# Kernel tuning notes

Measured on AMD Instinct MI355X. Metric: run time of the kernel, lower is better.

The kernel has to match this reference:

```python
import jax, jax.numpy as jnp
import numpy as np

N_A = 3
N_CLS = 80
IGNORE_THRE = 0.6
EPS = 1e-7


def _pairwise_iou_cxcywh(a, b):
    # a: [..., M, 4], b: [..., N, 4] in (cx, cy, w, h) -> IoU [..., M, N]
    a_xy, a_wh = a[..., :, None, :2], a[..., :, None, 2:4]
    b_xy, b_wh = b[..., None, :, :2], b[..., None, :, 2:4]
    tl = jnp.maximum(a_xy - a_wh * 0.5, b_xy - b_wh * 0.5)
    br = jnp.minimum(a_xy + a_wh * 0.5, b_xy + b_wh * 0.5)
    inter = jnp.prod(jnp.clip(br - tl, 0.0), axis=-1)
    area_a = a_wh[..., 0] * a_wh[..., 1]
    area_b = b_wh[..., 0] * b_wh[..., 1]
    return inter / jnp.maximum(area_a + area_b - inter, 1e-16)


def _bce(p, t):
    p = jnp.clip(p, EPS, 1.0 - EPS)
    return -(t * jnp.log(p) + (1.0 - t) * jnp.log(1.0 - p))


def _yolo_loss(raw, labels, anchors_all, anchor_indices, img_size):
    nB = raw.shape[0]
    nG = raw.shape[2]
    nCH = 5 + N_CLS
    K = labels.shape[1]
    sg = jax.lax.stop_gradient

    # decode raw: (B, A*CH, G, G) -> (B, A, G, G, CH)
    raw = jnp.transpose(raw.reshape(nB, N_A, nCH, nG, nG), (0, 1, 3, 4, 2))
    xy_offset = jax.nn.sigmoid(raw[..., 0:2])            # (B,A,G,G,2)
    wh_scale = raw[..., 2:4]                             # (B,A,G,G,2)
    conf = jax.nn.sigmoid(raw[..., 4])                   # (B,A,G,G)
    classes = jax.nn.sigmoid(raw[..., 5:])               # (B,A,G,G,ncls)

    anchors = anchors_all[anchor_indices]                # (3,2), pixels
    g = jnp.arange(nG, dtype=raw.dtype)
    xs = g[None, None, None, :]
    ys = g[None, None, :, None]

    # detached decoded predictions, normalized to [0,1]
    px = (sg(xy_offset[..., 0]) + xs) / nG
    py = (sg(xy_offset[..., 1]) + ys) / nG
    pw = jnp.minimum(jnp.exp(sg(wh_scale[..., 0])) * anchors[:, 0][None, :, None, None] / img_size, 1.0)
    ph = jnp.minimum(jnp.exp(sg(wh_scale[..., 1])) * anchors[:, 1][None, :, None, None] / img_size, 1.0)
    pred_boxes = jnp.stack([px, py, pw, ph], axis=-1).reshape(nB, -1, 4)  # (B, A*G*G, 4)

    # labels: (B, K, 5) = [cls, xc, yc, w, h]; targets are constants
    labels = sg(labels)
    nlabel = jnp.sum(jnp.sum(labels, axis=2) > 0, axis=1)                 # (B,)
    valid_k = jnp.arange(K)[None, :] < nlabel[:, None]                    # (B,K)
    tcls = labels[..., 0].astype(jnp.int32)
    tx = labels[..., 1] * nG
    ty = labels[..., 2] * nG
    tw = labels[..., 3]
    th = labels[..., 4]
    ti = tx.astype(jnp.int32)
    tj = ty.astype(jnp.int32)

    # anchor matching on centered (0,0,w,h) boxes against all 9 anchors
    anch00 = jnp.concatenate([jnp.zeros_like(anchors_all), anchors_all / img_size], axis=1)  # (9,4)
    gt00 = jnp.stack([jnp.zeros_like(tw), jnp.zeros_like(tw), tw, th], axis=-1)              # (B,K,4)
    a_ious = _pairwise_iou_cxcywh(gt00, anch00[None])                                        # (B,K,9)
    best_n_all = jnp.argmax(a_ious, axis=-1)                                                 # (B,K)
    valid_anchor = jnp.any(best_n_all[..., None] == anchor_indices[None, None, :], axis=-1)
    valid = valid_k & valid_anchor                                                           # (B,K)
    best_n = best_n_all % N_A

    # ignore mask: preds whose best IoU against any (valid) gt exceeds threshold
    gt_boxes = jnp.stack([tx / nG, ty / nG, tw, th], axis=-1) * valid_k[..., None].astype(raw.dtype)
    pred_ious = _pairwise_iou_cxcywh(pred_boxes, gt_boxes)               # (B, A*G*G, K)
    ignore = (jnp.max(pred_ious, axis=-1) > IGNORE_THRE).reshape(nB, N_A, nG, nG)
    penalty_mask = ~ignore

    # scatter gt assignments; invalid rows dropped via OOB batch index
    b_idx = jnp.broadcast_to(jnp.arange(nB)[:, None], (nB, K))
    b_s = jnp.where(valid, b_idx, nB)

    obj_mask = jnp.zeros((nB, N_A, nG, nG), dtype=bool).at[b_s, best_n, tj, ti].set(True, mode='drop')
    penalty_mask = penalty_mask.at[b_s, best_n, tj, ti].set(True, mode='drop')

    naw = anchors / img_size                                             # (3,2)
    tgt_vals = jnp.stack([
        tx - jnp.floor(tx),
        ty - jnp.floor(ty),
        jnp.log(tw / naw[best_n, 0] + 1e-16),
        jnp.log(th / naw[best_n, 1] + 1e-16),
    ], axis=-1)                                                          # (B,K,4)
    target4 = jnp.zeros((nB, N_A, nG, nG, 4), raw.dtype).at[b_s, best_n, tj, ti].set(tgt_vals, mode='drop')
    tgt_scale = jnp.zeros((nB, N_A, nG, nG), raw.dtype).at[b_s, best_n, tj, ti].set(
        jnp.sqrt(2.0 - tw * th), mode='drop')
    tcls_oh = jnp.zeros((nB, N_A, nG, nG, N_CLS), raw.dtype).at[b_s, best_n, tj, ti, tcls].set(1.0, mode='drop')

    obj_f = obj_mask.astype(raw.dtype)
    pen_f = penalty_mask.astype(raw.dtype)
    w2 = tgt_scale * tgt_scale                                           # (B,A,G,G)

    loss_xy = jnp.sum(obj_f[..., None] * w2[..., None] * _bce(xy_offset, target4[..., 0:2]))
    loss_wh = jnp.sum(obj_f[..., None] * w2[..., None] * jnp.square(wh_scale - target4[..., 2:4]))
    loss_obj = jnp.sum(pen_f * _bce(conf, obj_f))
    loss_cls = jnp.sum(obj_f[..., None] * _bce(classes, tcls_oh))
    return loss_xy + 0.5 * loss_wh + loss_obj + loss_cls


def setup_inputs() -> dict:
    key = jax.random.key(0)
    k1, k2, k3, k4 = jax.random.split(key, 4)
    nB, K, nG = 16, 50, 76
    raw = jax.random.normal(k1, (nB, N_A * (5 + N_CLS), nG, nG), jnp.float32) * 0.5
    cls = jax.random.randint(k2, (nB, K), 0, N_CLS).astype(jnp.float32)
    xy = jax.random.uniform(k3, (nB, K, 2), jnp.float32, 0.02, 0.98)
    wh = jax.random.uniform(k4, (nB, K, 2), jnp.float32, 0.02, 0.4)
    labels = jnp.concatenate([cls[..., None], xy, wh], axis=-1)
    # make per-image label counts < K (rows of zeros are "no label")
    labels = labels * (jnp.arange(K) < 40).astype(jnp.float32)[None, :, None]
    anchors_all = jnp.array([[10, 13], [16, 30], [33, 23], [30, 61], [62, 45],
                             [59, 119], [116, 90], [156, 198], [373, 326]], jnp.float32)
    anchor_indices = jnp.array([0, 1, 2], jnp.int32)
    return {"raw": raw, "labels": labels, "anchors_all": anchors_all,
            "anchor_indices": anchor_indices, "img_size": 608}


def reference(raw, labels, anchors_all, anchor_indices, img_size):
    return _yolo_loss(raw, labels, anchors_all, anchor_indices, img_size)
```

## Files before the change

kernel.cpp:

```cpp
#include <hip/hip_runtime.h>
#include <math.h>

#define NB   16
#define KL   50
#define NG   76
#define NA   3
#define NCLS 80
#define NCH  85
#define GG   (NG*NG)
#define CELLS (NA*GG)
#define LOSS_BX ((CELLS + 255) / 256)
#define NPART (LOSS_BX * NB)

__device__ __forceinline__ float softplusf(float x) {
    float t = __expf(-fabsf(x));
    return fmaxf(x, 0.0f) + __logf(1.0f + t);
}

__global__ __launch_bounds__(256) void yolo_fused(
    const float* __restrict__ raw,
    const float* __restrict__ labels,
    const float* __restrict__ anchors_all,
    const int*   __restrict__ anchor_indices,
    const int*   __restrict__ img_size_p,
    float* __restrict__ partials)
{
    const int b = blockIdx.y;

    __shared__ float4 s_box[KL];
    __shared__ float  s_c[KL];
    __shared__ int    s_meta[KL];
    __shared__ float  s_tgt[KL][4];
    __shared__ float  s_w2[KL];
    __shared__ int    s_tc[KL];
    __shared__ float  s_red[4];

    const float img = (float)img_size_p[0];
    const float inv_img = __builtin_amdgcn_rcpf(img);

    if (threadIdx.x < 64) {
        const int k = threadIdx.x;
        int has = 0;
        float cls = 0.f, tx = 0.f, ty = 0.f, tw = 0.f, th = 0.f;
        if (k < KL) {
            const float* L = labels + ((size_t)b * KL + k) * 5;
            cls = L[0];
            tw = L[3]; th = L[4];
            has = ((cls + L[1] + L[2] + tw + th) > 0.0f) ? 1 : 0;
            tx = L[1] * (float)NG;
            ty = L[2] * (float)NG;
        }
        unsigned long long bal = __ballot(has);
        int nlabel = __popcll(bal);

        if (k < KL) {
            int valid_k = (k < nlabel) ? 1 : 0;

            float best = -1.0f; int bestn = 0;
            float area_t = tw * th;
            for (int n = 0; n < 9; ++n) {
                float aw = anchors_all[2 * n + 0] * inv_img;
                float ah = anchors_all[2 * n + 1] * inv_img;
                float inter = fmaxf(fminf(tw, aw), 0.0f) * fmaxf(fminf(th, ah), 0.0f);
                float iou = inter / fmaxf(area_t + aw * ah - inter, 1e-16f);
                if (iou > best) { best = iou; bestn = n; }
            }
            int va = 0;
            for (int t = 0; t < 3; ++t) va |= (bestn == anchor_indices[t]) ? 1 : 0;
            int bn = bestn % NA;
            int ti = (int)tx, tj = (int)ty;
            int valid = valid_k && va && (ti >= 0) && (ti < NG) && (tj >= 0) && (tj < NG);
            s_meta[k] = valid ? (bn * GG + tj * NG + ti) : -1;

            float vkf = valid_k ? 1.0f : 0.0f;
            float gx = tx * (1.0f / (float)NG) * vkf;
            float gy = ty * (1.0f / (float)NG) * vkf;
            float gw = tw * vkf, gh = th * vkf;
            s_box[k] = make_float4(gx - 0.5f * gw, gy - 0.5f * gh,
                                   gx + 0.5f * gw, gy + 0.5f * gh);
            s_c[k] = 0.375f * (gw * gh);

            float naw = anchors_all[anchor_indices[bn] * 2 + 0] * inv_img;
            float nah = anchors_all[anchor_indices[bn] * 2 + 1] * inv_img;
            s_tgt[k][0] = tx - floorf(tx);
            s_tgt[k][1] = ty - floorf(ty);
            s_tgt[k][2] = __logf(tw / naw + 1e-16f);
            s_tgt[k][3] = __logf(th / nah + 1e-16f);
            s_w2[k] = 2.0f - tw * th;
            s_tc[k] = (int)cls;
        }
    }
    __syncthreads();

    const int c0 = blockIdx.x * 256 + threadIdx.x;
    const bool live = c0 < CELLS;
    const int c = live ? c0 : 0;

    const int a = c / GG;
    const int r = c - a * GG;
    const int j = r / NG;
    const int i = r - j * NG;
    const float* R = raw + ((size_t)(b * NA + a) * NCH) * GG + r;

    float rx = R[0],      ry = R[GG];
    float rw = R[2 * GG], rh = R[3 * GG];
    float rc = R[4 * GG];

    float sx = __builtin_amdgcn_rcpf(1.0f + __expf(-rx));
    float sy = __builtin_amdgcn_rcpf(1.0f + __expf(-ry));

    int ai = anchor_indices[a];
    float aw = anchors_all[2 * ai + 0] * inv_img;
    float ah = anchors_all[2 * ai + 1] * inv_img;

    float px = (sx + (float)i) * (1.0f / (float)NG);
    float py = (sy + (float)j) * (1.0f / (float)NG);
    float pw = fminf(__expf(rw) * aw, 1.0f);
    float ph = fminf(__expf(rh) * ah, 1.0f);

    float tA = 0.375f * (pw * ph);
    float ax0 = px - 0.5f * pw, ax1 = px + 0.5f * pw;
    float ay0 = py - 0.5f * ph, ay1 = py + 0.5f * ph;

    float margin = -1.0f;
    int kobj = -1;
    #pragma unroll 10
    for (int k = 0; k < KL; ++k) {
        float4 g = s_box[k];
        float iw = fminf(ax1, g.z) - fmaxf(ax0, g.x);
        float ih = fminf(ay1, g.w) - fmaxf(ay0, g.y);
        float inter = fmaxf(iw, 0.0f) * fmaxf(ih, 0.0f);
        margin = fmaxf(margin, inter - s_c[k]);
        kobj = (s_meta[k] == c) ? k : kobj;
    }
    bool ignore = margin > tA;
    bool obj = (kobj >= 0) && live;

    float loss = 0.0f;
    if (obj || !ignore)
        loss = softplusf(rc) - (obj ? rc : 0.0f);

    if (obj) {
        float w2 = s_w2[kobj];
        float t0 = s_tgt[kobj][0], t1 = s_tgt[kobj][1];
        float t2 = s_tgt[kobj][2], t3 = s_tgt[kobj][3];
        loss += w2 * ((softplusf(rx) - t0 * rx) + (softplusf(ry) - t1 * ry));
        float dw = rw - t2, dh = rh - t3;
        loss += 0.5f * w2 * (dw * dw + dh * dh);
        int tc = s_tc[kobj];
        float cl = 0.0f;
        #pragma unroll 8
        for (int cc = 0; cc < NCLS; ++cc) {
            float z = R[(5 + cc) * GG];
            cl += softplusf(z);
            if (cc == tc) cl -= z;
        }
        loss += cl;
    }
    if (!live) loss = 0.0f;

    for (int off = 32; off > 0; off >>= 1)
        loss += __shfl_down(loss, off, 64);
    if ((threadIdx.x & 63) == 0) s_red[threadIdx.x >> 6] = loss;
    __syncthreads();
    if (threadIdx.x == 0)
        partials[(size_t)blockIdx.y * gridDim.x + blockIdx.x] =
            s_red[0] + s_red[1] + s_red[2] + s_red[3];
}

__global__ __launch_bounds__(256) void yolo_finalize(
    const float* __restrict__ partials, float* __restrict__ out)
{
    float s = 0.0f;
    for (int i = threadIdx.x; i < NPART; i += 256) s += partials[i];
    for (int off = 32; off > 0; off >>= 1)
        s += __shfl_down(s, off, 64);
    __shared__ float red[4];
    if ((threadIdx.x & 63) == 0) red[threadIdx.x >> 6] = s;
    __syncthreads();
    if (threadIdx.x == 0) out[0] = red[0] + red[1] + red[2] + red[3];
}

extern "C" void kernel_launch(void* const* d_in, const int* in_sizes, int n_in,
                              void* d_out, int out_size, void* d_ws, size_t ws_size,
                              hipStream_t stream) {
    const float* raw            = (const float*)d_in[0];
    const float* labels         = (const float*)d_in[1];
    const float* anchors_all    = (const float*)d_in[2];
    const int*   anchor_indices = (const int*)d_in[3];
    const int*   img_size_p     = (const int*)d_in[4];
    float* out = (float*)d_out;

    float* partials = (float*)d_ws;

    dim3 grid(LOSS_BX, NB);
    yolo_fused<<<grid, 256, 0, stream>>>(raw, labels, anchors_all,
                                         anchor_indices, img_size_p, partials);
    yolo_finalize<<<1, 256, 0, stream>>>(partials, out);
}
```

Measured before the change: 142.5 us.

## Process four cells per thread with float4 loads and 64-thread blocks

Each thread now handles four consecutive grid cells, loading the box and confidence channels as float4 vectors and reusing each shared-memory label read across four cells in the IoU loop. Blocks shrink to a single 64-lane wavefront, so the label preprocessing runs on every thread and the cross-wave shared reduction and its barrier go away. The intent is fewer LDS reads per cell and wider global loads. In exchange, per-thread register use rises, and the class-loss loop for object cells still reads channels with strided scalar loads. Because GG (5776) is a multiple of 4, the float4 loads stay aligned and four consecutive cells never cross an anchor plane.

```diff
diff --git a/kernel.cpp b/kernel.cpp
--- a/kernel.cpp
+++ b/kernel.cpp
@@ -9,7 +9,10 @@
 #define NCH  85
 #define GG   (NG*NG)
 #define CELLS (NA*GG)
-#define LOSS_BX ((CELLS + 255) / 256)
+#define CPT  4
+#define TPB  64
+#define CPB  (TPB*CPT)
+#define LOSS_BX ((CELLS + CPB - 1) / CPB)
 #define NPART (LOSS_BX * NB)
 
 __device__ __forceinline__ float softplusf(float x) {
@@ -17,7 +20,7 @@
     return fmaxf(x, 0.0f) + __logf(1.0f + t);
 }
 
-__global__ __launch_bounds__(256) void yolo_fused(
+__global__ __launch_bounds__(64) void yolo_fused(
     const float* __restrict__ raw,
     const float* __restrict__ labels,
     const float* __restrict__ anchors_all,
@@ -30,15 +33,14 @@
     __shared__ float4 s_box[KL];
     __shared__ float  s_c[KL];
     __shared__ int    s_meta[KL];
-    __shared__ float  s_tgt[KL][4];
+    __shared__ float4 s_tgt[KL];
     __shared__ float  s_w2[KL];
     __shared__ int    s_tc[KL];
-    __shared__ float  s_red[4];
 
     const float img = (float)img_size_p[0];
     const float inv_img = __builtin_amdgcn_rcpf(img);
 
-    if (threadIdx.x < 64) {
+    {
         const int k = threadIdx.x;
         int has = 0;
         float cls = 0.f, tx = 0.f, ty = 0.f, tw = 0.f, th = 0.f;
@@ -82,90 +84,106 @@
 
             float naw = anchors_all[anchor_indices[bn] * 2 + 0] * inv_img;
             float nah = anchors_all[anchor_indices[bn] * 2 + 1] * inv_img;
-            s_tgt[k][0] = tx - floorf(tx);
-            s_tgt[k][1] = ty - floorf(ty);
-            s_tgt[k][2] = __logf(tw / naw + 1e-16f);
-            s_tgt[k][3] = __logf(th / nah + 1e-16f);
+            s_tgt[k] = make_float4(tx - floorf(tx), ty - floorf(ty),
+                                   __logf(tw / naw + 1e-16f),
+                                   __logf(th / nah + 1e-16f));
             s_w2[k] = 2.0f - tw * th;
             s_tc[k] = (int)cls;
         }
     }
     __syncthreads();
 
-    const int c0 = blockIdx.x * 256 + threadIdx.x;
+    const int c0 = blockIdx.x * CPB + threadIdx.x * CPT;
     const bool live = c0 < CELLS;
-    const int c = live ? c0 : 0;
-
-    const int a = c / GG;
-    const int r = c - a * GG;
+    const int cb = live ? c0 : 0;
+
+    const int a = cb / GG;
+    const int r = cb - a * GG;
     const int j = r / NG;
     const int i = r - j * NG;
     const float* R = raw + ((size_t)(b * NA + a) * NCH) * GG + r;
 
-    float rx = R[0],      ry = R[GG];
-    float rw = R[2 * GG], rh = R[3 * GG];
-    float rc = R[4 * GG];
-
-    float sx = __builtin_amdgcn_rcpf(1.0f + __expf(-rx));
-    float sy = __builtin_amdgcn_rcpf(1.0f + __expf(-ry));
+    float4 rx4 = *(const float4*)(R);
+    float4 ry4 = *(const float4*)(R + GG);
+    float4 rw4 = *(const float4*)(R + 2 * GG);
+    float4 rh4 = *(const float4*)(R + 3 * GG);
+    float4 rc4 = *(const float4*)(R + 4 * GG);
 
     int ai = anchor_indices[a];
     float aw = anchors_all[2 * ai + 0] * inv_img;
     float ah = anchors_all[2 * ai + 1] * inv_img;
 
-    float px = (sx + (float)i) * (1.0f / (float)NG);
-    float py = (sy + (float)j) * (1.0f / (float)NG);
-    float pw = fminf(__expf(rw) * aw, 1.0f);
-    float ph = fminf(__expf(rh) * ah, 1.0f);
-
-    float tA = 0.375f * (pw * ph);
-    float ax0 = px - 0.5f * pw, ax1 = px + 0.5f * pw;
-    float ay0 = py - 0.5f * ph, ay1 = py + 0.5f * ph;
-
-    float margin = -1.0f;
-    int kobj = -1;
-    #pragma unroll 10
+    float rxv[CPT] = {rx4.x, rx4.y, rx4.z, rx4.w};
+    float ryv[CPT] = {ry4.x, ry4.y, ry4.z, ry4.w};
+    float rwv[CPT] = {rw4.x, rw4.y, rw4.z, rw4.w};
+    float rhv[CPT] = {rh4.x, rh4.y, rh4.z, rh4.w};
+    float rcv[CPT] = {rc4.x, rc4.y, rc4.z, rc4.w};
+
+    float ax0[CPT], ax1[CPT], ay0[CPT], ay1[CPT], tA[CPT], margin[CPT];
+    int kobj[CPT];
+    #pragma unroll
+    for (int cc = 0; cc < CPT; ++cc) {
+        float sx = __builtin_amdgcn_rcpf(1.0f + __expf(-rxv[cc]));
+        float sy = __builtin_amdgcn_rcpf(1.0f + __expf(-ryv[cc]));
+        float px = (sx + (float)(i + cc)) * (1.0f / (float)NG);
+        float py = (sy + (float)j) * (1.0f / (float)NG);
+        float pw = fminf(__expf(rwv[cc]) * aw, 1.0f);
+        float ph = fminf(__expf(rhv[cc]) * ah, 1.0f);
+        tA[cc] = 0.375f * (pw * ph);
+        ax0[cc] = px - 0.5f * pw; ax1[cc] = px + 0.5f * pw;
+        ay0[cc] = py - 0.5f * ph; ay1[cc] = py + 0.5f * ph;
+        margin[cc] = -1.0f;
+        kobj[cc] = -1;
+    }
+
+    #pragma unroll 5
     for (int k = 0; k < KL; ++k) {
         float4 g = s_box[k];
-        float iw = fminf(ax1, g.z) - fmaxf(ax0, g.x);
-        float ih = fminf(ay1, g.w) - fmaxf(ay0, g.y);
-        float inter = fmaxf(iw, 0.0f) * fmaxf(ih, 0.0f);
-        margin = fmaxf(margin, inter - s_c[k]);
-        kobj = (s_meta[k] == c) ? k : kobj;
-    }
-    bool ignore = margin > tA;
-    bool obj = (kobj >= 0) && live;
+        float cB = s_c[k];
+        int   mk = s_meta[k];
+        #pragma unroll
+        for (int cc = 0; cc < CPT; ++cc) {
+            float iw = fminf(ax1[cc], g.z) - fmaxf(ax0[cc], g.x);
+            float ih = fminf(ay1[cc], g.w) - fmaxf(ay0[cc], g.y);
+            float inter = fmaxf(iw, 0.0f) * fmaxf(ih, 0.0f);
+            margin[cc] = fmaxf(margin[cc], inter - cB);
+            kobj[cc] = (mk == cb + cc) ? k : kobj[cc];
+        }
+    }
 
     float loss = 0.0f;
-    if (obj || !ignore)
-        loss = softplusf(rc) - (obj ? rc : 0.0f);
-
-    if (obj) {
-        float w2 = s_w2[kobj];
-        float t0 = s_tgt[kobj][0], t1 = s_tgt[kobj][1];
-        float t2 = s_tgt[kobj][2], t3 = s_tgt[kobj][3];
-        loss += w2 * ((softplusf(rx) - t0 * rx) + (softplusf(ry) - t1 * ry));
-        float dw = rw - t2, dh = rh - t3;
-        loss += 0.5f * w2 * (dw * dw + dh * dh);
-        int tc = s_tc[kobj];
-        float cl = 0.0f;
-        #pragma unroll 8
-        for (int cc = 0; cc < NCLS; ++cc) {
-            float z = R[(5 + cc) * GG];
-            cl += softplusf(z);
-            if (cc == tc) cl -= z;
-        }
-        loss += cl;
+    #pragma unroll
+    for (int cc = 0; cc < CPT; ++cc) {
+        bool ignore = margin[cc] > tA[cc];
+        bool obj = kobj[cc] >= 0;
+
+        if (obj || !ignore)
+            loss += softplusf(rcv[cc]) - (obj ? rcv[cc] : 0.0f);
+
+        if (obj) {
+            float4 t = s_tgt[kobj[cc]];
+            float w2 = s_w2[kobj[cc]];
+            loss += w2 * ((softplusf(rxv[cc]) - t.x * rxv[cc]) +
+                          (softplusf(ryv[cc]) - t.y * ryv[cc]));
+            float dw = rwv[cc] - t.z, dh = rhv[cc] - t.w;
+            loss += 0.5f * w2 * (dw * dw + dh * dh);
+            int tc = s_tc[kobj[cc]];
+            float cl = 0.0f;
+            #pragma unroll 8
+            for (int ch = 0; ch < NCLS; ++ch) {
+                float z = R[(5 + ch) * GG + cc];
+                cl += softplusf(z);
+                if (ch == tc) cl -= z;
+            }
+            loss += cl;
+        }
     }
     if (!live) loss = 0.0f;
 
     for (int off = 32; off > 0; off >>= 1)
         loss += __shfl_down(loss, off, 64);
-    if ((threadIdx.x & 63) == 0) s_red[threadIdx.x >> 6] = loss;
-    __syncthreads();
     if (threadIdx.x == 0)
-        partials[(size_t)blockIdx.y * gridDim.x + blockIdx.x] =
-            s_red[0] + s_red[1] + s_red[2] + s_red[3];
+        partials[(size_t)b * LOSS_BX + blockIdx.x] = loss;
 }
 
 __global__ __launch_bounds__(256) void yolo_finalize(
@@ -194,7 +212,7 @@
     float* partials = (float*)d_ws;
 
     dim3 grid(LOSS_BX, NB);
-    yolo_fused<<<grid, 256, 0, stream>>>(raw, labels, anchors_all,
+    yolo_fused<<<grid, TPB, 0, stream>>>(raw, labels, anchors_all,
                                          anchor_indices, img_size_p, partials);
     yolo_finalize<<<1, 256, 0, stream>>>(partials, out);
 }
```

Result: slower. 146.8 us (+3.0%).
